# Kernel optimization log

Hardware: AMD Instinct MI355X
Metric: run time of the kernel (lower is better)

The kernel has to match this reference:

```python
import jax, jax.numpy as jnp
import numpy as np

N_FEATURES = 1024
N_HEADS = 16
DEPTH = N_FEATURES // N_HEADS


def setup_inputs() -> dict:
    key = jax.random.key(0)
    ks = jax.random.split(key, 12)
    B, S, D = 2, 2048, N_FEATURES
    s = 1.0 / np.sqrt(D)
    return {
        "q": jax.random.normal(ks[0], (B, S, D), jnp.float32),
        "k": jax.random.normal(ks[1], (B, S, D), jnp.float32),
        "v": jax.random.normal(ks[2], (B, S, D), jnp.float32),
        "w_q": jax.random.normal(ks[3], (D, D), jnp.float32) * s,
        "b_q": jnp.zeros((D,), jnp.float32),
        "w_k": jax.random.normal(ks[4], (D, D), jnp.float32) * s,
        "b_k": jnp.zeros((D,), jnp.float32),
        "w_v": jax.random.normal(ks[5], (D, D), jnp.float32) * s,
        "b_v": jnp.zeros((D,), jnp.float32),
        "w_o": jax.random.normal(ks[6], (D, D), jnp.float32) * s,
        "b_o": jnp.zeros((D,), jnp.float32),
    }


def _split_heads(x):
    # [B, S, D] -> [B, H, S, depth]
    B, S, _ = x.shape
    return x.reshape(B, S, N_HEADS, DEPTH).transpose(0, 2, 1, 3)


def reference(q, k, v, w_q, b_q, w_k, b_k, w_v, b_v, w_o, b_o):
    B, S, D = q.shape
    qh = _split_heads(q @ w_q + b_q)  # [B,H,S,d]
    kh = _split_heads(k @ w_k + b_k)
    vh = _split_heads(v @ w_v + b_v)
    scale = 1.0 / jnp.sqrt(jnp.asarray(DEPTH, jnp.float32))
    logits = jnp.einsum("bhqd,bhkd->bhqk", qh, kh) * scale  # [B,H,S,S]
    attn_weights = jax.nn.softmax(logits, axis=-1)
    attn = jnp.einsum("bhqk,bhkd->bhqd", attn_weights, vh)
    concat = attn.transpose(0, 2, 1, 3).reshape(B, S, D)
    output = concat @ w_o + b_o
    return output, attn_weights
```

## Files before the change

### kernel.cpp

```cpp
#include <hip/hip_runtime.h>

typedef __attribute__((ext_vector_type(8))) short short8;
typedef __attribute__((ext_vector_type(4))) float f32x4;

#define MFMA_BF16(A,B,C) __builtin_amdgcn_mfma_f32_16x16x32_bf16((A),(B),(C),0,0,0)

#define SCALE_LOG2E 0.18033688011112043f

__device__ __forceinline__ unsigned short f2bu(float f) {
  unsigned int u = __float_as_uint(f);
  u += 0x7fffu + ((u >> 16) & 1u);
  return (unsigned short)(u >> 16);
}
__device__ __forceinline__ float bu2f(unsigned short u) {
  return __uint_as_float(((unsigned int)u) << 16);
}
__device__ __forceinline__ void gload16(const void* g, void* l) {
  __builtin_amdgcn_global_load_lds(
      (const __attribute__((address_space(1))) void*)g,
      (__attribute__((address_space(3))) void*)l, 16, 0, 0);
}
#define WAITV0 asm volatile("s_waitcnt vmcnt(0)" ::: "memory")
#define WAITV4 asm volatile("s_waitcnt vmcnt(4)" ::: "memory")
__device__ __forceinline__ void barrier_fence() {
  __builtin_amdgcn_s_barrier();
  __builtin_amdgcn_sched_barrier(0);
}

struct Cvt3Args { const float* s[3]; unsigned short* d[3]; };
__global__ __launch_bounds__(256) void cvt3_kernel(Cvt3Args a) {
  const int w = blockIdx.y;
  int i = blockIdx.x * 256 + threadIdx.x;
  const float4 v = reinterpret_cast<const float4*>(a.s[w])[i];
  ushort4 o;
  o.x = f2bu(v.x); o.y = f2bu(v.y); o.z = f2bu(v.z); o.w = f2bu(v.w);
  reinterpret_cast<ushort4*>(a.d[w])[i] = o;
}

struct Tr4Args { const float* s[4]; unsigned short* d[4]; };
__global__ __launch_bounds__(256) void transpose4_kernel(Tr4Args a) {
  __shared__ float t[32][33];
  const float* w = a.s[blockIdx.z];
  unsigned short* wt = a.d[blockIdx.z];
  const int bx = blockIdx.x * 32;
  const int by = blockIdx.y * 32;
  const int tx = threadIdx.x & 31, ty = threadIdx.x >> 5;
  for (int j = 0; j < 4; ++j)
    t[ty + 8 * j][tx] = w[(size_t)(bx + ty + 8 * j) * 1024 + by + tx];
  __syncthreads();
  for (int j = 0; j < 4; ++j)
    wt[(size_t)(by + ty + 8 * j) * 1024 + bx + tx] = f2bu(t[tx][ty + 8 * j]);
}

template <int OUT_MODE>
__global__ __launch_bounds__(512) void gemm_bt(
    const unsigned short* __restrict__ A, const unsigned short* __restrict__ Wt,
    const float* __restrict__ bias, void* __restrict__ Cout) {
  __shared__ unsigned short g_lds[2][16384];
  const int M0 = blockIdx.x * 128, N0 = blockIdx.y * 128;
  const int tid = threadIdx.x, lane = tid & 63, wid = tid >> 6;
  const int lr = lane & 15, lg = lane >> 4;
  const int wr = wid >> 2, wc = wid & 3;
  const int srow = lane >> 3, slot = lane & 7;
  f32x4 acc[4][2];
#pragma unroll
  for (int m = 0; m < 4; ++m)
#pragma unroll
    for (int n = 0; n < 2; ++n) acc[m][n] = (f32x4){0.f, 0.f, 0.f, 0.f};

#define G_STAGE(buf, kk)                                                             \
  {                                                                                  \
    _Pragma("unroll") for (int i_ = 0; i_ < 2; ++i_) {                               \
      int idx_ = wid * 2 + i_;                                                       \
      int row_ = idx_ * 8 + srow;                                                    \
      int gs_ = slot ^ (row_ & 7);                                                   \
      gload16(&A[(size_t)(M0 + row_) * 1024 + (kk) + gs_ * 8],                       \
              (char*)&g_lds[buf][0] + idx_ * 1024);                                  \
      gload16(&Wt[(size_t)(N0 + row_) * 1024 + (kk) + gs_ * 8],                      \
              (char*)&g_lds[buf][0] + 16384 + idx_ * 1024);                          \
    }                                                                                \
  }

  G_STAGE(0, 0);
  __syncthreads();
  for (int kt = 0; kt < 16; ++kt) {
    const int cur = kt & 1;
    if (kt < 15) G_STAGE(cur ^ 1, (kt + 1) * 64);
    short8 af[4][2], bf[2][2];
#pragma unroll
    for (int m = 0; m < 4; ++m)
#pragma unroll
      for (int kh = 0; kh < 2; ++kh) {
        int row = wr * 64 + m * 16 + lr;
        int s = (kh * 4 + lg) ^ (row & 7);
        af[m][kh] = *reinterpret_cast<const short8*>((const char*)&g_lds[cur][0] + row * 128 + s * 16);
      }
#pragma unroll
    for (int n = 0; n < 2; ++n)
#pragma unroll
      for (int kh = 0; kh < 2; ++kh) {
        int row = wc * 32 + n * 16 + lr;
        int s = (kh * 4 + lg) ^ (row & 7);
        bf[n][kh] = *reinterpret_cast<const short8*>((const char*)&g_lds[cur][0] + 16384 + row * 128 + s * 16);
      }
#pragma unroll
    for (int kh = 0; kh < 2; ++kh)
#pragma unroll
      for (int m = 0; m < 4; ++m)
#pragma unroll
        for (int n = 0; n < 2; ++n)
          acc[m][n] = MFMA_BF16(af[m][kh], bf[n][kh], acc[m][n]);
    __syncthreads();
  }

  if (OUT_MODE != 2) {
#pragma unroll
    for (int m = 0; m < 4; ++m)
#pragma unroll
      for (int n = 0; n < 2; ++n)
#pragma unroll
        for (int r = 0; r < 4; ++r) {
          int grow = M0 + wr * 64 + m * 16 + lg * 4 + r;
          int gcol = N0 + wc * 32 + n * 16 + lr;
          float vv = acc[m][n][r] + bias[gcol];
          if (OUT_MODE == 1)
            reinterpret_cast<float*>(Cout)[(size_t)grow * 1024 + gcol] = vv;
          else
            reinterpret_cast<unsigned short*>(Cout)[(size_t)grow * 1024 + gcol] = f2bu(vv);
        }
  } else {
    unsigned short* t = &g_lds[0][0];
#pragma unroll
    for (int m = 0; m < 4; ++m)
#pragma unroll
      for (int n = 0; n < 2; ++n) {
        int ch = wc * 32 + n * 16 + lr;
        int s4 = wr * 64 + m * 16 + lg * 4;
        int sb = (s4 * 2) ^ ((ch & 7) << 4);
        ushort4 pk;
        pk.x = f2bu(acc[m][n][0] + bias[N0 + ch]);
        pk.y = f2bu(acc[m][n][1] + bias[N0 + ch]);
        pk.z = f2bu(acc[m][n][2] + bias[N0 + ch]);
        pk.w = f2bu(acc[m][n][3] + bias[N0 + ch]);
        *reinterpret_cast<ushort4*>((char*)t + ch * 256 + sb) = pk;
      }
    __syncthreads();
    unsigned short* Vt = (unsigned short*)Cout;
    const int ch = tid >> 2, sc = tid & 3;
    const int bb = M0 >> 11;
    unsigned short* dst = Vt + (size_t)(bb * 1024 + N0 + ch) * 2048 + (M0 & 2047) + sc * 8;
#pragma unroll
    for (int i = 0; i < 4; ++i) {
      int sb = (sc * 16 + i * 64) ^ ((ch & 7) << 4);
      short8 v = *reinterpret_cast<const short8*>((const char*)t + ch * 256 + sb);
      *reinterpret_cast<short8*>(dst + i * 32) = v;
    }
  }
#undef G_STAGE
}

__global__ __launch_bounds__(512) void attn_kernel(
    const unsigned short* __restrict__ Qp, const unsigned short* __restrict__ Kp,
    const unsigned short* __restrict__ Vt, float* __restrict__ attnw,
    unsigned short* __restrict__ attnc) {
  __shared__ unsigned short k_lds[2][4096];
  __shared__ unsigned short vt_lds[2][4096];
  __shared__ unsigned short w_lds[8][16][68];
  __shared__ float linv_lds[128];
  const int bid = blockIdx.x;
  const int qt = bid & 15, h = (bid >> 4) & 15, b = bid >> 8;
  const int tid = threadIdx.x, lane = tid & 63, wid = tid >> 6;
  const int lr = lane & 15, lg = lane >> 4;
  const int q0 = qt * 128;
  const int srow = lane >> 3, slot = lane & 7;

  short8 aq[2];
#pragma unroll
  for (int kh = 0; kh < 2; ++kh)
    aq[kh] = *reinterpret_cast<const short8*>(
        &Qp[(size_t)(b * 2048 + q0 + wid * 16 + lr) * 1024 + h * 64 + kh * 32 + lg * 8]);

  const size_t kbase = (size_t)b * 2048 * 1024 + (size_t)(h * 64);
  const size_t vtbase = (size_t)(b * 1024 + h * 64) * 2048;

#define K_STAGE(buf, kk)                                                          \
  {                                                                               \
    int row_ = wid * 8 + srow;                                                    \
    int gs_ = slot ^ (row_ & 7);                                                  \
    gload16(&Kp[kbase + (size_t)((kk) + row_) * 1024 + gs_ * 8],                  \
            (char*)&k_lds[buf][0] + wid * 1024);                                  \
  }
#define V_STAGE(buf, kk)                                                          \
  {                                                                               \
    int row_ = wid * 8 + srow;                                                    \
    int gs_ = slot ^ (row_ & 7);                                                  \
    gload16(&Vt[vtbase + (size_t)row_ * 2048 + (kk) + gs_ * 8],                   \
            (char*)&vt_lds[buf][0] + wid * 1024);                                 \
  }

  float lsum[4] = {0.f, 0.f, 0.f, 0.f};

  K_STAGE(0, 0);
  for (int kt = 0; kt < 32; ++kt) {
    const int cur = kt & 1;
    WAITV0;
    barrier_fence();
    if (kt < 31) K_STAGE(cur ^ 1, (kt + 1) * 64);
    f32x4 lacc[4];
#pragma unroll
    for (int nt = 0; nt < 4; ++nt) lacc[nt] = (f32x4){0.f, 0.f, 0.f, 0.f};
#pragma unroll
    for (int kh = 0; kh < 2; ++kh)
#pragma unroll
      for (int nt = 0; nt < 4; ++nt) {
        int row = nt * 16 + lr;
        int s = (kh * 4 + lg) ^ (row & 7);
        short8 kb = *reinterpret_cast<const short8*>((const char*)&k_lds[cur][0] + row * 128 + s * 16);
        lacc[nt] = MFMA_BF16(aq[kh], kb, lacc[nt]);
      }
#pragma unroll
    for (int nt = 0; nt < 4; ++nt)
#pragma unroll
      for (int r = 0; r < 4; ++r)
        lsum[r] += exp2f(lacc[nt][r] * SCALE_LOG2E);
  }
  float invl[4];
#pragma unroll
  for (int r = 0; r < 4; ++r) {
    float s = lsum[r];
    s += __shfl_xor(s, 1); s += __shfl_xor(s, 2);
    s += __shfl_xor(s, 4); s += __shfl_xor(s, 8);
    float inv = 1.f / s;
    invl[r] = inv;
    if (lr == 0) linv_lds[wid * 16 + lg * 4 + r] = inv;
  }
  float inv_j[4];
#pragma unroll
  for (int j = 0; j < 4; ++j) inv_j[j] = linv_lds[wid * 16 + 4 * j + lg];

  f32x4 oacc[4];
#pragma unroll
  for (int nt = 0; nt < 4; ++nt) oacc[nt] = (f32x4){0.f, 0.f, 0.f, 0.f};

  const size_t wrowb = (size_t)((b * 16 + h) * 2048) + q0 + wid * 16;

  __syncthreads();

  K_STAGE(0, 0);
  V_STAGE(0, 0);
  for (int kt = 0; kt < 32; ++kt) {
    const int cur = kt & 1;
    const int k0 = kt * 64;
    if (kt == 0) { WAITV0; } else { WAITV4; }
    barrier_fence();
    if (kt < 31) { K_STAGE(cur ^ 1, k0 + 64); V_STAGE(cur ^ 1, k0 + 64); }
    f32x4 lacc[4];
#pragma unroll
    for (int nt = 0; nt < 4; ++nt) lacc[nt] = (f32x4){0.f, 0.f, 0.f, 0.f};
#pragma unroll
    for (int kh = 0; kh < 2; ++kh)
#pragma unroll
      for (int nt = 0; nt < 4; ++nt) {
        int row = nt * 16 + lr;
        int s = (kh * 4 + lg) ^ (row & 7);
        short8 kb = *reinterpret_cast<const short8*>((const char*)&k_lds[cur][0] + row * 128 + s * 16);
        lacc[nt] = MFMA_BF16(aq[kh], kb, lacc[nt]);
      }
#pragma unroll
    for (int nt = 0; nt < 4; ++nt)
#pragma unroll
      for (int r = 0; r < 4; ++r)
        w_lds[wid][lg * 4 + r][nt * 16 + lr] = f2bu(exp2f(lacc[nt][r] * SCALE_LOG2E));
#pragma unroll
    for (int ks = 0; ks < 2; ++ks) {
      short8 wa = *reinterpret_cast<const short8*>(&w_lds[wid][lr][ks * 32 + lg * 8]);
#pragma unroll
      for (int nt = 0; nt < 4; ++nt) {
        int row = nt * 16 + lr;
        int s = (ks * 4 + lg) ^ (row & 7);
        short8 vb = *reinterpret_cast<const short8*>((const char*)&vt_lds[cur][0] + row * 128 + s * 16);
        oacc[nt] = MFMA_BF16(wa, vb, oacc[nt]);
      }
    }
#pragma unroll
    for (int j = 0; j < 4; ++j) {
      int rowl = 4 * j + lg;
      ushort4 wv = *reinterpret_cast<const ushort4*>(&w_lds[wid][rowl][lr * 4]);
      f32x4 o;
      o[0] = bu2f(wv.x) * inv_j[j];
      o[1] = bu2f(wv.y) * inv_j[j];
      o[2] = bu2f(wv.z) * inv_j[j];
      o[3] = bu2f(wv.w) * inv_j[j];
      __builtin_nontemporal_store(o, reinterpret_cast<f32x4*>(&attnw[(wrowb + rowl) * 2048 + k0 + lr * 4]));
    }
  }
#pragma unroll
  for (int nt = 0; nt < 4; ++nt)
#pragma unroll
    for (int r = 0; r < 4; ++r) {
      int srow2 = q0 + wid * 16 + lg * 4 + r;
      attnc[(size_t)(b * 2048 + srow2) * 1024 + h * 64 + nt * 16 + lr] =
          f2bu(oacc[nt][r] * invl[r]);
    }
#undef K_STAGE
#undef V_STAGE
}

extern "C" void kernel_launch(void* const* d_in, const int* in_sizes, int n_in,
                              void* d_out, int out_size, void* d_ws, size_t ws_size,
                              hipStream_t stream) {
  const float* q = (const float*)d_in[0];
  const float* k = (const float*)d_in[1];
  const float* v = (const float*)d_in[2];
  const float* w_q = (const float*)d_in[3];
  const float* b_q = (const float*)d_in[4];
  const float* w_k = (const float*)d_in[5];
  const float* b_k = (const float*)d_in[6];
  const float* w_v = (const float*)d_in[7];
  const float* b_v = (const float*)d_in[8];
  const float* w_o = (const float*)d_in[9];
  const float* b_o = (const float*)d_in[10];

  unsigned short* ws = (unsigned short*)d_ws;
  unsigned short* Qp    = ws;
  unsigned short* Kp    = ws + 4194304;
  unsigned short* Vt    = ws + 8388608;
  unsigned short* attnc = ws + 12582912;
  unsigned short* wqt = ws + 16777216;
  unsigned short* wkt = wqt + 1048576;
  unsigned short* wvt = wkt + 1048576;
  unsigned short* wot = wvt + 1048576;

  float* outO = (float*)d_out;
  float* attnw = outO + 4194304;

  unsigned short* qb = (unsigned short*)attnw;
  unsigned short* kb = qb + 4194304;
  unsigned short* vb = kb + 4194304;

  Tr4Args ta;
  ta.s[0] = w_q; ta.s[1] = w_k; ta.s[2] = w_v; ta.s[3] = w_o;
  ta.d[0] = wqt; ta.d[1] = wkt; ta.d[2] = wvt; ta.d[3] = wot;
  transpose4_kernel<<<dim3(32, 32, 4), 256, 0, stream>>>(ta);

  Cvt3Args ca;
  ca.s[0] = q; ca.s[1] = k; ca.s[2] = v;
  ca.d[0] = qb; ca.d[1] = kb; ca.d[2] = vb;
  cvt3_kernel<<<dim3(4096, 3), 256, 0, stream>>>(ca);

  gemm_bt<0><<<dim3(32, 8), 512, 0, stream>>>(qb, wqt, b_q, (void*)Qp);
  gemm_bt<0><<<dim3(32, 8), 512, 0, stream>>>(kb, wkt, b_k, (void*)Kp);
  gemm_bt<2><<<dim3(32, 8), 512, 0, stream>>>(vb, wvt, b_v, (void*)Vt);

  attn_kernel<<<512, 512, 0, stream>>>(Qp, Kp, Vt, attnw, attnc);

  gemm_bt<1><<<dim3(32, 8), 512, 0, stream>>>(attnc, wot, b_o, d_out);
}
```

Measured before the change: 244.2 us.

## Merge prep and QKV GEMM launches, split attention into denominator and PV kernels

Combines the weight transpose and input conversion into one prep kernel, and batches the three QKV projection GEMMs into one launch with a z-dimension. The attention kernel is split into a row-sum denominator kernel, which uses 128-wide K tiles, and a PV/weights kernel that reads the precomputed inverse sums. Both attention kernels remap block indices so that consecutive blocks land on different heads. The goal is fewer launches, more parallelism per launch and shorter per-block serial work. The cost is a second read of Q and K across kernels, and the inverse sums are stored in the wqt buffer, which is dead by then.

```diff
diff --git a/kernel.cpp b/kernel.cpp
--- a/kernel.cpp
+++ b/kernel.cpp
@@ -27,37 +27,39 @@
   __builtin_amdgcn_sched_barrier(0);
 }
 
-struct Cvt3Args { const float* s[3]; unsigned short* d[3]; };
-__global__ __launch_bounds__(256) void cvt3_kernel(Cvt3Args a) {
-  const int w = blockIdx.y;
-  int i = blockIdx.x * 256 + threadIdx.x;
-  const float4 v = reinterpret_cast<const float4*>(a.s[w])[i];
-  ushort4 o;
-  o.x = f2bu(v.x); o.y = f2bu(v.y); o.z = f2bu(v.z); o.w = f2bu(v.w);
-  reinterpret_cast<ushort4*>(a.d[w])[i] = o;
-}
-
-struct Tr4Args { const float* s[4]; unsigned short* d[4]; };
-__global__ __launch_bounds__(256) void transpose4_kernel(Tr4Args a) {
+struct PrepArgs {
+  const float* src[7];
+  unsigned short* dst[7];
+};
+__global__ __launch_bounds__(256) void prep_kernel(PrepArgs a) {
   __shared__ float t[32][33];
-  const float* w = a.s[blockIdx.z];
-  unsigned short* wt = a.d[blockIdx.z];
-  const int bx = blockIdx.x * 32;
-  const int by = blockIdx.y * 32;
-  const int tx = threadIdx.x & 31, ty = threadIdx.x >> 5;
-  for (int j = 0; j < 4; ++j)
-    t[ty + 8 * j][tx] = w[(size_t)(bx + ty + 8 * j) * 1024 + by + tx];
-  __syncthreads();
-  for (int j = 0; j < 4; ++j)
-    wt[(size_t)(by + ty + 8 * j) * 1024 + bx + tx] = f2bu(t[tx][ty + 8 * j]);
+  if (blockIdx.y < 3) {
+    const int w = blockIdx.y;
+    const int i = blockIdx.x * 256 + threadIdx.x;
+    const float4 v = reinterpret_cast<const float4*>(a.src[w])[i];
+    ushort4 o;
+    o.x = f2bu(v.x); o.y = f2bu(v.y); o.z = f2bu(v.z); o.w = f2bu(v.w);
+    reinterpret_cast<ushort4*>(a.dst[w])[i] = o;
+  } else {
+    const int m = blockIdx.x >> 10;
+    const float* w = a.src[3 + m];
+    unsigned short* wt = a.dst[3 + m];
+    const int bx = ((blockIdx.x >> 5) & 31) * 32;
+    const int by = (blockIdx.x & 31) * 32;
+    const int tx = threadIdx.x & 31, ty = threadIdx.x >> 5;
+    for (int j = 0; j < 4; ++j)
+      t[ty + 8 * j][tx] = w[(size_t)(bx + ty + 8 * j) * 1024 + by + tx];
+    __syncthreads();
+    for (int j = 0; j < 4; ++j)
+      wt[(size_t)(by + ty + 8 * j) * 1024 + bx + tx] = f2bu(t[tx][ty + 8 * j]);
+  }
 }
 
 template <int OUT_MODE>
-__global__ __launch_bounds__(512) void gemm_bt(
+__device__ __forceinline__ void gemm_core(
+    unsigned short* g_lds,
     const unsigned short* __restrict__ A, const unsigned short* __restrict__ Wt,
-    const float* __restrict__ bias, void* __restrict__ Cout) {
-  __shared__ unsigned short g_lds[2][16384];
-  const int M0 = blockIdx.x * 128, N0 = blockIdx.y * 128;
+    const float* __restrict__ bias, void* __restrict__ Cout, int M0, int N0) {
   const int tid = threadIdx.x, lane = tid & 63, wid = tid >> 6;
   const int lr = lane & 15, lg = lane >> 4;
   const int wr = wid >> 2, wc = wid & 3;
@@ -75,9 +77,9 @@
       int row_ = idx_ * 8 + srow;                                                    \
       int gs_ = slot ^ (row_ & 7);                                                   \
       gload16(&A[(size_t)(M0 + row_) * 1024 + (kk) + gs_ * 8],                       \
-              (char*)&g_lds[buf][0] + idx_ * 1024);                                  \
+              (char*)g_lds + (buf) * 32768 + idx_ * 1024);                           \
       gload16(&Wt[(size_t)(N0 + row_) * 1024 + (kk) + gs_ * 8],                      \
-              (char*)&g_lds[buf][0] + 16384 + idx_ * 1024);                          \
+              (char*)g_lds + (buf) * 32768 + 16384 + idx_ * 1024);                   \
     }                                                                                \
   }
 
@@ -93,7 +95,7 @@
       for (int kh = 0; kh < 2; ++kh) {
         int row = wr * 64 + m * 16 + lr;
         int s = (kh * 4 + lg) ^ (row & 7);
-        af[m][kh] = *reinterpret_cast<const short8*>((const char*)&g_lds[cur][0] + row * 128 + s * 16);
+        af[m][kh] = *reinterpret_cast<const short8*>((const char*)g_lds + cur * 32768 + row * 128 + s * 16);
       }
 #pragma unroll
     for (int n = 0; n < 2; ++n)
@@ -101,7 +103,7 @@
       for (int kh = 0; kh < 2; ++kh) {
         int row = wc * 32 + n * 16 + lr;
         int s = (kh * 4 + lg) ^ (row & 7);
-        bf[n][kh] = *reinterpret_cast<const short8*>((const char*)&g_lds[cur][0] + 16384 + row * 128 + s * 16);
+        bf[n][kh] = *reinterpret_cast<const short8*>((const char*)g_lds + cur * 32768 + 16384 + row * 128 + s * 16);
       }
 #pragma unroll
     for (int kh = 0; kh < 2; ++kh)
@@ -129,7 +131,7 @@
             reinterpret_cast<unsigned short*>(Cout)[(size_t)grow * 1024 + gcol] = f2bu(vv);
         }
   } else {
-    unsigned short* t = &g_lds[0][0];
+    unsigned short* t = g_lds;
 #pragma unroll
     for (int m = 0; m < 4; ++m)
 #pragma unroll
@@ -159,15 +161,31 @@
 #undef G_STAGE
 }
 
-__global__ __launch_bounds__(512) void attn_kernel(
+struct Gemm3Args {
+  const unsigned short* A[3]; const unsigned short* Wt[3];
+  const float* bias[3]; void* C[3];
+};
+__global__ __launch_bounds__(512) void gemm3_kernel(Gemm3Args a) {
+  __shared__ unsigned short g_lds[2 * 16384];
+  const int z = blockIdx.z;
+  if (z == 2)
+    gemm_core<2>(g_lds, a.A[2], a.Wt[2], a.bias[2], a.C[2], blockIdx.x * 128, blockIdx.y * 128);
+  else
+    gemm_core<0>(g_lds, a.A[z], a.Wt[z], a.bias[z], a.C[z], blockIdx.x * 128, blockIdx.y * 128);
+}
+
+__global__ __launch_bounds__(512) void gemm_out_kernel(
+    const unsigned short* __restrict__ A, const unsigned short* __restrict__ Wt,
+    const float* __restrict__ bias, float* __restrict__ C) {
+  __shared__ unsigned short g_lds[2 * 16384];
+  gemm_core<1>(g_lds, A, Wt, bias, C, blockIdx.x * 128, blockIdx.y * 128);
+}
+
+__global__ __launch_bounds__(512) void attn_den_kernel(
     const unsigned short* __restrict__ Qp, const unsigned short* __restrict__ Kp,
-    const unsigned short* __restrict__ Vt, float* __restrict__ attnw,
-    unsigned short* __restrict__ attnc) {
-  __shared__ unsigned short k_lds[2][4096];
-  __shared__ unsigned short vt_lds[2][4096];
-  __shared__ unsigned short w_lds[8][16][68];
-  __shared__ float linv_lds[128];
-  const int bid = blockIdx.x;
+    float* __restrict__ invl_g) {
+  __shared__ unsigned short k_lds[2][8192];
+  const int bid = ((blockIdx.x & 7) << 6) | (blockIdx.x >> 3);
   const int qt = bid & 15, h = (bid >> 4) & 15, b = bid >> 8;
   const int tid = threadIdx.x, lane = tid & 63, wid = tid >> 6;
   const int lr = lane & 15, lg = lane >> 4;
@@ -179,6 +197,82 @@
   for (int kh = 0; kh < 2; ++kh)
     aq[kh] = *reinterpret_cast<const short8*>(
         &Qp[(size_t)(b * 2048 + q0 + wid * 16 + lr) * 1024 + h * 64 + kh * 32 + lg * 8]);
+
+  const size_t kbase = (size_t)b * 2048 * 1024 + (size_t)(h * 64);
+
+#define KD_STAGE(buf, kk)                                                         \
+  {                                                                               \
+    _Pragma("unroll") for (int i_ = 0; i_ < 2; ++i_) {                            \
+      int idx_ = wid * 2 + i_;                                                    \
+      int row_ = idx_ * 8 + srow;                                                 \
+      int gs_ = slot ^ (row_ & 7);                                                \
+      gload16(&Kp[kbase + (size_t)((kk) + row_) * 1024 + gs_ * 8],                \
+              (char*)&k_lds[buf][0] + idx_ * 1024);                               \
+    }                                                                             \
+  }
+
+  float lsum[4] = {0.f, 0.f, 0.f, 0.f};
+
+  KD_STAGE(0, 0);
+  WAITV0;
+  barrier_fence();
+  for (int kt = 0; kt < 16; ++kt) {
+    const int cur = kt & 1;
+    if (kt < 15) KD_STAGE(cur ^ 1, (kt + 1) * 128);
+    f32x4 lacc[8];
+#pragma unroll
+    for (int nt = 0; nt < 8; ++nt) lacc[nt] = (f32x4){0.f, 0.f, 0.f, 0.f};
+#pragma unroll
+    for (int kh = 0; kh < 2; ++kh)
+#pragma unroll
+      for (int nt = 0; nt < 8; ++nt) {
+        int row = nt * 16 + lr;
+        int s = (kh * 4 + lg) ^ (row & 7);
+        short8 kb = *reinterpret_cast<const short8*>((const char*)&k_lds[cur][0] + row * 128 + s * 16);
+        lacc[nt] = MFMA_BF16(aq[kh], kb, lacc[nt]);
+      }
+#pragma unroll
+    for (int nt = 0; nt < 8; ++nt)
+#pragma unroll
+      for (int r = 0; r < 4; ++r)
+        lsum[r] += exp2f(lacc[nt][r] * SCALE_LOG2E);
+    WAITV0;
+    barrier_fence();
+  }
+#pragma unroll
+  for (int r = 0; r < 4; ++r) {
+    float s = lsum[r];
+    s += __shfl_xor(s, 1); s += __shfl_xor(s, 2);
+    s += __shfl_xor(s, 4); s += __shfl_xor(s, 8);
+    if (lr == 0) invl_g[bid * 128 + wid * 16 + lg * 4 + r] = 1.f / s;
+  }
+#undef KD_STAGE
+}
+
+__global__ __launch_bounds__(512) void attn_pv_kernel(
+    const unsigned short* __restrict__ Qp, const unsigned short* __restrict__ Kp,
+    const unsigned short* __restrict__ Vt, const float* __restrict__ invl_g,
+    float* __restrict__ attnw, unsigned short* __restrict__ attnc) {
+  __shared__ unsigned short k_lds[2][4096];
+  __shared__ unsigned short vt_lds[2][4096];
+  __shared__ unsigned short w_lds[8][16][68];
+  const int bid = ((blockIdx.x & 7) << 6) | (blockIdx.x >> 3);
+  const int qt = bid & 15, h = (bid >> 4) & 15, b = bid >> 8;
+  const int tid = threadIdx.x, lane = tid & 63, wid = tid >> 6;
+  const int lr = lane & 15, lg = lane >> 4;
+  const int q0 = qt * 128;
+  const int srow = lane >> 3, slot = lane & 7;
+
+  short8 aq[2];
+#pragma unroll
+  for (int kh = 0; kh < 2; ++kh)
+    aq[kh] = *reinterpret_cast<const short8*>(
+        &Qp[(size_t)(b * 2048 + q0 + wid * 16 + lr) * 1024 + h * 64 + kh * 32 + lg * 8]);
+
+  const f32x4 invl = *reinterpret_cast<const f32x4*>(&invl_g[bid * 128 + wid * 16 + lg * 4]);
+  float inv_j[4];
+#pragma unroll
+  for (int j = 0; j < 4; ++j) inv_j[j] = invl_g[bid * 128 + wid * 16 + 4 * j + lg];
 
   const size_t kbase = (size_t)b * 2048 * 1024 + (size_t)(h * 64);
   const size_t vtbase = (size_t)(b * 1024 + h * 64) * 2048;
@@ -198,61 +292,19 @@
             (char*)&vt_lds[buf][0] + wid * 1024);                                 \
   }
 
-  float lsum[4] = {0.f, 0.f, 0.f, 0.f};
-
-  K_STAGE(0, 0);
-  for (int kt = 0; kt < 32; ++kt) {
-    const int cur = kt & 1;
-    WAITV0;
-    barrier_fence();
-    if (kt < 31) K_STAGE(cur ^ 1, (kt + 1) * 64);
-    f32x4 lacc[4];
-#pragma unroll
-    for (int nt = 0; nt < 4; ++nt) lacc[nt] = (f32x4){0.f, 0.f, 0.f, 0.f};
-#pragma unroll
-    for (int kh = 0; kh < 2; ++kh)
-#pragma unroll
-      for (int nt = 0; nt < 4; ++nt) {
-        int row = nt * 16 + lr;
-        int s = (kh * 4 + lg) ^ (row & 7);
-        short8 kb = *reinterpret_cast<const short8*>((const char*)&k_lds[cur][0] + row * 128 + s * 16);
-        lacc[nt] = MFMA_BF16(aq[kh], kb, lacc[nt]);
-      }
-#pragma unroll
-    for (int nt = 0; nt < 4; ++nt)
-#pragma unroll
-      for (int r = 0; r < 4; ++r)
-        lsum[r] += exp2f(lacc[nt][r] * SCALE_LOG2E);
-  }
-  float invl[4];
-#pragma unroll
-  for (int r = 0; r < 4; ++r) {
-    float s = lsum[r];
-    s += __shfl_xor(s, 1); s += __shfl_xor(s, 2);
-    s += __shfl_xor(s, 4); s += __shfl_xor(s, 8);
-    float inv = 1.f / s;
-    invl[r] = inv;
-    if (lr == 0) linv_lds[wid * 16 + lg * 4 + r] = inv;
-  }
-  float inv_j[4];
-#pragma unroll
-  for (int j = 0; j < 4; ++j) inv_j[j] = linv_lds[wid * 16 + 4 * j + lg];
-
   f32x4 oacc[4];
 #pragma unroll
   for (int nt = 0; nt < 4; ++nt) oacc[nt] = (f32x4){0.f, 0.f, 0.f, 0.f};
 
   const size_t wrowb = (size_t)((b * 16 + h) * 2048) + q0 + wid * 16;
-
-  __syncthreads();
 
   K_STAGE(0, 0);
   V_STAGE(0, 0);
+  WAITV0;
+  barrier_fence();
   for (int kt = 0; kt < 32; ++kt) {
     const int cur = kt & 1;
     const int k0 = kt * 64;
-    if (kt == 0) { WAITV0; } else { WAITV4; }
-    barrier_fence();
     if (kt < 31) { K_STAGE(cur ^ 1, k0 + 64); V_STAGE(cur ^ 1, k0 + 64); }
     f32x4 lacc[4];
 #pragma unroll
@@ -293,6 +345,8 @@
       o[3] = bu2f(wv.w) * inv_j[j];
       __builtin_nontemporal_store(o, reinterpret_cast<f32x4*>(&attnw[(wrowb + rowl) * 2048 + k0 + lr * 4]));
     }
+    WAITV4;
+    barrier_fence();
   }
 #pragma unroll
   for (int nt = 0; nt < 4; ++nt)
@@ -330,6 +384,7 @@
   unsigned short* wkt = wqt + 1048576;
   unsigned short* wvt = wkt + 1048576;
   unsigned short* wot = wvt + 1048576;
+  float* invl_g = (float*)wqt;
 
   float* outO = (float*)d_out;
   float* attnw = outO + 4194304;
@@ -338,21 +393,22 @@
   unsigned short* kb = qb + 4194304;
   unsigned short* vb = kb + 4194304;
 
-  Tr4Args ta;
-  ta.s[0] = w_q; ta.s[1] = w_k; ta.s[2] = w_v; ta.s[3] = w_o;
-  ta.d[0] = wqt; ta.d[1] = wkt; ta.d[2] = wvt; ta.d[3] = wot;
-  transpose4_kernel<<<dim3(32, 32, 4), 256, 0, stream>>>(ta);
-
-  Cvt3Args ca;
-  ca.s[0] = q; ca.s[1] = k; ca.s[2] = v;
-  ca.d[0] = qb; ca.d[1] = kb; ca.d[2] = vb;
-  cvt3_kernel<<<dim3(4096, 3), 256, 0, stream>>>(ca);
-
-  gemm_bt<0><<<dim3(32, 8), 512, 0, stream>>>(qb, wqt, b_q, (void*)Qp);
-  gemm_bt<0><<<dim3(32, 8), 512, 0, stream>>>(kb, wkt, b_k, (void*)Kp);
-  gemm_bt<2><<<dim3(32, 8), 512, 0, stream>>>(vb, wvt, b_v, (void*)Vt);
-
-  attn_kernel<<<512, 512, 0, stream>>>(Qp, Kp, Vt, attnw, attnc);
-
-  gemm_bt<1><<<dim3(32, 8), 512, 0, stream>>>(attnc, wot, b_o, d_out);
-}
+  PrepArgs pa;
+  pa.src[0] = q; pa.src[1] = k; pa.src[2] = v;
+  pa.src[3] = w_q; pa.src[4] = w_k; pa.src[5] = w_v; pa.src[6] = w_o;
+  pa.dst[0] = qb; pa.dst[1] = kb; pa.dst[2] = vb;
+  pa.dst[3] = wqt; pa.dst[4] = wkt; pa.dst[5] = wvt; pa.dst[6] = wot;
+  prep_kernel<<<dim3(4096, 4), 256, 0, stream>>>(pa);
+
+  Gemm3Args ga;
+  ga.A[0] = qb; ga.A[1] = kb; ga.A[2] = vb;
+  ga.Wt[0] = wqt; ga.Wt[1] = wkt; ga.Wt[2] = wvt;
+  ga.bias[0] = b_q; ga.bias[1] = b_k; ga.bias[2] = b_v;
+  ga.C[0] = Qp; ga.C[1] = Kp; ga.C[2] = Vt;
+  gemm3_kernel<<<dim3(32, 8, 3), 512, 0, stream>>>(ga);
+
+  attn_den_kernel<<<512, 512, 0, stream>>>(Qp, Kp, invl_g);
+  attn_pv_kernel<<<512, 512, 0, stream>>>(Qp, Kp, Vt, invl_g, attnw, attnc);
+
+  gemm_out_kernel<<<dim3(32, 8), 512, 0, stream>>>(attnc, wot, b_o, outO);
+}
```

Result: faster. 229.3 us (-6.1%).
